# Optimization experiments

Measured on AMD Instinct MI355X. Metric: run time of the kernel, lower is better.

## Reference

```python
import jax, jax.numpy as jnp
import numpy as np
from jax import lax

D_MODEL = 1024
D_STATE = 16
D_CONV = 4
EXPAND = 2
D_INNER = EXPAND * D_MODEL          # 2048
DT_RANK = (D_MODEL + 15) // 16      # 64
FF_INNER = 4 * D_MODEL              # 4096
B, L = 2, 2048
EPS = 1e-5


def _layer_norm(x, g, b):
    mu = jnp.mean(x, axis=-1, keepdims=True)
    var = jnp.mean(jnp.square(x - mu), axis=-1, keepdims=True)
    return (x - mu) * lax.rsqrt(var + EPS) * g + b


def setup_inputs() -> dict:
    key = jax.random.key(0)
    ks = jax.random.split(key, 10)
    def n(k, shape, s=0.02):
        return jax.random.normal(k, shape, dtype=jnp.float32) * s
    x = jax.random.normal(ks[0], (B, L, D_MODEL), dtype=jnp.float32)
    return dict(
        x=x,
        ln1_g=jnp.ones((D_MODEL,), jnp.float32), ln1_b=jnp.zeros((D_MODEL,), jnp.float32),
        w_in=n(ks[1], (D_MODEL, 2 * D_INNER)),
        conv_w=n(ks[2], (D_INNER, D_CONV), 0.2), conv_b=jnp.zeros((D_INNER,), jnp.float32),
        w_x=n(ks[3], (D_INNER, DT_RANK + 2 * D_STATE)),
        w_dt=n(ks[4], (DT_RANK, D_INNER), 0.1),
        b_dt=jnp.full((D_INNER,), -4.6, jnp.float32),  # softplus(-4.6) ~= 0.01 dt init
        a_log=jnp.log(jnp.broadcast_to(jnp.arange(1, D_STATE + 1, dtype=jnp.float32), (D_INNER, D_STATE))),
        d_skip=jnp.ones((D_INNER,), jnp.float32),
        w_out=n(ks[5], (D_INNER, D_MODEL)),
        ln2_g=jnp.ones((D_MODEL,), jnp.float32), ln2_b=jnp.zeros((D_MODEL,), jnp.float32),
        w_ff1=n(ks[6], (D_MODEL, 2 * FF_INNER)), b_ff1=jnp.zeros((2 * FF_INNER,), jnp.float32),
        w_ff2=n(ks[7], (FF_INNER, D_MODEL)), b_ff2=jnp.zeros((D_MODEL,), jnp.float32),
    )


def _mamba(h, w_in, conv_w, conv_b, w_x, w_dt, b_dt, a_log, d_skip, w_out):
    # h: (B, L, D_MODEL)
    xz = h @ w_in                                   # (B, L, 2*D_INNER)
    xc, z = jnp.split(xz, 2, axis=-1)               # each (B, L, D_INNER)
    # depthwise causal conv1d along L
    xc_t = jnp.transpose(xc, (0, 2, 1))             # (B, D_INNER, L)
    xc_t = lax.conv_general_dilated(
        xc_t, conv_w[:, None, :], window_strides=(1,), padding=[(D_CONV - 1, 0)],
        feature_group_count=D_INNER, dimension_numbers=('NCH', 'OIH', 'NCH'))
    xc = jnp.transpose(xc_t, (0, 2, 1)) + conv_b
    xc = jax.nn.silu(xc)
    # input-dependent dt, B, C
    dbc = xc @ w_x                                  # (B, L, DT_RANK+2*D_STATE)
    dt_lo, Bm, Cm = jnp.split(dbc, [DT_RANK, DT_RANK + D_STATE], axis=-1)
    dt = jax.nn.softplus(dt_lo @ w_dt + b_dt)       # (B, L, D_INNER)
    A = -jnp.exp(a_log)                             # (D_INNER, D_STATE)

    def step(hst, inp):
        dt_t, B_t, C_t, x_t = inp                   # (B,di),(B,N),(B,N),(B,di)
        dA = jnp.exp(dt_t[..., None] * A)           # (B, D_INNER, D_STATE)
        hst = hst * dA + (dt_t * x_t)[..., None] * B_t[:, None, :]
        y = jnp.einsum('bdn,bn->bd', hst, C_t)
        return hst, y

    h0 = jnp.zeros((h.shape[0], D_INNER, D_STATE), dt.dtype)
    xs = (jnp.swapaxes(dt, 0, 1), jnp.swapaxes(Bm, 0, 1),
          jnp.swapaxes(Cm, 0, 1), jnp.swapaxes(xc, 0, 1))
    _, ys = lax.scan(step, h0, xs)                  # ys: (L, B, D_INNER)
    y = jnp.swapaxes(ys, 0, 1) + d_skip * xc
    y = y * jax.nn.silu(z)
    return y @ w_out                                # (B, L, D_MODEL)


def _geglu_ff(h, w1, b1, w2, b2):
    p = h @ w1 + b1
    a, g = jnp.split(p, 2, axis=-1)
    return (a * jax.nn.gelu(g)) @ w2 + b2


def reference(x, ln1_g, ln1_b, w_in, conv_w, conv_b, w_x, w_dt, b_dt, a_log,
              d_skip, w_out, ln2_g, ln2_b, w_ff1, b_ff1, w_ff2, b_ff2):
    h = _layer_norm(x, ln1_g, ln1_b)
    x = x + _mamba(h, w_in, conv_w, conv_b, w_x, w_dt, b_dt, a_log, d_skip, w_out)
    h2 = _layer_norm(x, ln2_g, ln2_b)
    x = x + _geglu_ff(h2, w_ff1, b_ff1, w_ff2, b_ff2)
    return x
```

## Files before the change

kernel.cpp:

```cpp
#include <hip/hip_runtime.h>
#include <hip/hip_bf16.h>
#include <stdint.h>
#include <stddef.h>


typedef __bf16 bf16;
typedef __bf16 bf16x8 __attribute__((ext_vector_type(8)));
typedef float  f32x4  __attribute__((ext_vector_type(4)));

static constexpr int kB  = 2;
static constexpr int kL  = 2048;
static constexpr int kDM = 1024;
static constexpr int kDI = 2048;
static constexpr int kM  = kB * kL;
static constexpr int kNC = 64;
static constexpr int kCH = kL / kNC;

__device__ __forceinline__ void gload16(const void* g, void* l) {
  __builtin_amdgcn_global_load_lds((__attribute__((address_space(1))) void*)g,
                                   (__attribute__((address_space(3))) void*)l,
                                   16, 0, 0);
}

__global__ __launch_bounds__(256) void transpose_to_bf16(
    const float* __restrict__ w, bf16* __restrict__ wt, int K, int N, int Npad) {
  __shared__ float t[32][33];
  const int k0 = blockIdx.x * 32, n0 = blockIdx.y * 32;
  const int tx = threadIdx.x & 31, ty = threadIdx.x >> 5;
#pragma unroll
  for (int i = ty; i < 32; i += 8) {
    float v = 0.f;
    if (k0 + i < K && n0 + tx < N) v = w[(size_t)(k0 + i) * N + n0 + tx];
    t[i][tx] = v;
  }
  __syncthreads();
#pragma unroll
  for (int i = ty; i < 32; i += 8) {
    const int n = n0 + i, k = k0 + tx;
    if (n < Npad && k < K) wt[(size_t)n * K + k] = (bf16)t[tx][i];
  }
}

__global__ __launch_bounds__(256) void layernorm_to_bf16(
    const float* __restrict__ x, const float* __restrict__ g,
    const float* __restrict__ b, bf16* __restrict__ out) {
  const int row = blockIdx.x;
  const float4 v = ((const float4*)(x + (size_t)row * kDM))[threadIdx.x];
  float s  = v.x + v.y + v.z + v.w;
  float s2 = v.x * v.x + v.y * v.y + v.z * v.z + v.w * v.w;
#pragma unroll
  for (int off = 1; off < 64; off <<= 1) {
    s  += __shfl_xor(s, off);
    s2 += __shfl_xor(s2, off);
  }
  __shared__ float ws[4], ws2[4];
  const int wave = threadIdx.x >> 6, lane = threadIdx.x & 63;
  if (lane == 0) { ws[wave] = s; ws2[wave] = s2; }
  __syncthreads();
  s  = ws[0] + ws[1] + ws[2] + ws[3];
  s2 = ws2[0] + ws2[1] + ws2[2] + ws2[3];
  const float mu  = s * (1.f / kDM);
  const float var = s2 * (1.f / kDM) - mu * mu;
  const float r   = rsqrtf(var + 1e-5f);
  const int c = threadIdx.x * 4;
  const float4 gg = ((const float4*)g)[threadIdx.x];
  const float4 bb = ((const float4*)b)[threadIdx.x];
  bf16* o = out + (size_t)row * kDM + c;
  o[0] = (bf16)((v.x - mu) * r * gg.x + bb.x);
  o[1] = (bf16)((v.y - mu) * r * gg.y + bb.y);
  o[2] = (bf16)((v.z - mu) * r * gg.z + bb.z);
  o[3] = (bf16)((v.w - mu) * r * gg.w + bb.w);
}

template <int MODE>
__global__ __launch_bounds__(256, 2) void gemm_bt(
    const bf16* __restrict__ A, int lda,
    const bf16* __restrict__ BT, int ldbt, int K,
    float* __restrict__ C0, bf16* __restrict__ C1,
    const float* __restrict__ bias, const float* __restrict__ res) {
  __shared__ __align__(16) bf16 As[128 * 32];
  __shared__ __align__(16) bf16 Bs[128 * 32];

  const int tid  = threadIdx.x;
  const int wave = tid >> 6;
  const int lane = tid & 63;
  const int m0 = blockIdx.y * 128;
  const int n0 = blockIdx.x * 128;
  const int wr = wave >> 1, wc = wave & 1;
  const int lr = lane & 15, kg = lane >> 4;

  const int srow = lane >> 2;
  const int scol = (lane & 3) * 8;

  const bf16* Ag0 = A  + (size_t)(m0 + wave * 32 + srow) * lda  + scol;
  const bf16* Ag1 = Ag0 + (size_t)16 * lda;
  const bf16* Bg0 = BT + (size_t)(n0 + wave * 32 + srow) * ldbt + scol;
  const bf16* Bg1 = Bg0 + (size_t)16 * ldbt;
  bf16* Al0 = As + wave * 1024;
  bf16* Al1 = Al0 + 512;
  bf16* Bl0 = Bs + wave * 1024;
  bf16* Bl1 = Bl0 + 512;

  f32x4 acc[4][4] = {};

  for (int kt = 0; kt < K; kt += 32) {
    __syncthreads();
    gload16(Ag0 + kt, Al0);
    gload16(Ag1 + kt, Al1);
    gload16(Bg0 + kt, Bl0);
    gload16(Bg1 + kt, Bl1);
    __syncthreads();

    bf16x8 af[4], bfr[4];
#pragma unroll
    for (int i = 0; i < 4; ++i) {
      af[i]  = *(const bf16x8*)(As + (wr * 64 + i * 16 + lr) * 32 + kg * 8);
      bfr[i] = *(const bf16x8*)(Bs + (wc * 64 + i * 16 + lr) * 32 + kg * 8);
    }
#pragma unroll
    for (int i = 0; i < 4; ++i)
#pragma unroll
      for (int j = 0; j < 4; ++j)
        acc[i][j] =
            __builtin_amdgcn_mfma_f32_16x16x32_bf16(af[i], bfr[j], acc[i][j], 0, 0, 0);
  }

#pragma unroll
  for (int i = 0; i < 4; ++i) {
    const int mbase = m0 + wr * 64 + i * 16 + kg * 4;
#pragma unroll
    for (int j = 0; j < 4; ++j) {
      const int n = n0 + wc * 64 + j * 16 + lr;
#pragma unroll
      for (int e = 0; e < 4; ++e) {
        const int m = mbase + e;
        const float v = acc[i][j][e];
        if constexpr (MODE == 0) {
          if (n < kDI) C0[(size_t)m * kDI + n] = v;
          else         C1[(size_t)m * kDI + (n - kDI)] = (bf16)(v / (1.f + expf(-v)));
        } else if constexpr (MODE == 1) {
          C0[(size_t)m * 128 + n] = v;
          if (n < 64) C1[(size_t)m * 64 + n] = (bf16)v;
        } else if constexpr (MODE == 2) {
          const float t = v + bias[n];
          const float sp = (t > 0.f) ? (t + log1pf(expf(-t))) : log1pf(expf(t));
          C0[(size_t)m * kDI + n] = sp;
        } else if constexpr (MODE == 3) {
          C0[(size_t)m * kDM + n] = v + res[(size_t)m * kDM + n];
        } else if constexpr (MODE == 4) {
          C1[(size_t)m * 8192 + n] = (bf16)(v + bias[n]);
        } else {
          C0[(size_t)m * kDM + n] = v + bias[n] + res[(size_t)m * kDM + n];
        }
      }
    }
  }
}

__global__ __launch_bounds__(256) void conv_silu(
    const float* __restrict__ xc_raw, const float* __restrict__ cw,
    const float* __restrict__ cb, float* __restrict__ xf, bf16* __restrict__ xb) {
  const int idx = blockIdx.x * 256 + threadIdx.x;
  const int d = idx & (kDI - 1);
  const int m = idx >> 11;
  const int l = m & (kL - 1);
  float acc = cb[d];
  const float w0 = cw[d * 4 + 0], w1 = cw[d * 4 + 1], w2 = cw[d * 4 + 2],
              w3 = cw[d * 4 + 3];
  if (l >= 3) acc += xc_raw[(size_t)(m - 3) * kDI + d] * w0;
  if (l >= 2) acc += xc_raw[(size_t)(m - 2) * kDI + d] * w1;
  if (l >= 1) acc += xc_raw[(size_t)(m - 1) * kDI + d] * w2;
  acc += xc_raw[(size_t)m * kDI + d] * w3;
  const float a = acc / (1.f + expf(-acc));
  xf[idx] = a;
  xb[idx] = (bf16)a;
}


__global__ __launch_bounds__(256) void scan_p1(
    const float* __restrict__ dt, const float* __restrict__ xc,
    const float* __restrict__ dbc, const float* __restrict__ a_log,
    float* __restrict__ P, float* __restrict__ Q) {
  const int dg = blockIdx.x & 7;
  const int c  = (blockIdx.x >> 3) & (kNC - 1);
  const int b  = blockIdx.x >> 9;
  const int d  = dg * 256 + threadIdx.x;
  __shared__ __align__(16) float BC[kCH][32];
  {
    const int l  = threadIdx.x >> 3;
    const int cg = (threadIdx.x & 7) * 4;
    *(float4*)&BC[l][cg] =
        *(const float4*)&dbc[(size_t)(b * kL + c * kCH + l) * 128 + 64 + cg];
  }
  __syncthreads();
  float A[16];
#pragma unroll
  for (int q = 0; q < 4; ++q) {
    const float4 al = *(const float4*)&a_log[d * 16 + q * 4];
    A[q * 4 + 0] = -__expf(al.x);
    A[q * 4 + 1] = -__expf(al.y);
    A[q * 4 + 2] = -__expf(al.z);
    A[q * 4 + 3] = -__expf(al.w);
  }
  float h[16] = {};
  float sdt = 0.f;
  const size_t rb = ((size_t)b * kL + c * kCH) * kDI + d;
#pragma unroll 2
  for (int l = 0; l < kCH; ++l) {
    const float dtv = dt[rb + (size_t)l * kDI];
    const float xv  = xc[rb + (size_t)l * kDI];
    const float u   = dtv * xv;
    sdt += dtv;
    float Bv[16];
    *(float4*)&Bv[0]  = *(const float4*)&BC[l][0];
    *(float4*)&Bv[4]  = *(const float4*)&BC[l][4];
    *(float4*)&Bv[8]  = *(const float4*)&BC[l][8];
    *(float4*)&Bv[12] = *(const float4*)&BC[l][12];
#pragma unroll
    for (int n = 0; n < 16; ++n) {
      const float dA = __expf(dtv * A[n]);
      h[n] = h[n] * dA + u * Bv[n];
    }
  }
  const size_t o = (((size_t)b * kNC + c) * kDI + d) * 16;
  float Pv[16];
#pragma unroll
  for (int n = 0; n < 16; ++n) Pv[n] = __expf(sdt * A[n]);
#pragma unroll
  for (int q = 0; q < 4; ++q) {
    *(float4*)&P[o + q * 4] = *(float4*)&Pv[q * 4];
    *(float4*)&Q[o + q * 4] = *(float4*)&h[q * 4];
  }
}

__global__ __launch_bounds__(256) void scan_p2(
    const float* __restrict__ P, const float* __restrict__ Q,
    float* __restrict__ H0) {
  const int i  = blockIdx.x * 256 + threadIdx.x;
  const int dn = i & (kDI * 16 - 1);
  const int b  = i >> 15;
  float h = 0.f;
#pragma unroll 8
  for (int c = 0; c < kNC; ++c) {
    const size_t idx = ((size_t)(b * kNC + c)) * (kDI * 16) + dn;
    H0[idx] = h;
    h = P[idx] * h + Q[idx];
  }
}

__global__ __launch_bounds__(256) void scan_p3(
    const float* __restrict__ dt, const float* __restrict__ xc,
    const float* __restrict__ dbc, const float* __restrict__ a_log,
    const float* __restrict__ d_skip, const bf16* __restrict__ zs,
    const float* __restrict__ H0, bf16* __restrict__ y) {
  const int dg = blockIdx.x & 7;
  const int c  = (blockIdx.x >> 3) & (kNC - 1);
  const int b  = blockIdx.x >> 9;
  const int d  = dg * 256 + threadIdx.x;
  __shared__ __align__(16) float BC[kCH][32];
  {
    const int l  = threadIdx.x >> 3;
    const int cg = (threadIdx.x & 7) * 4;
    *(float4*)&BC[l][cg] =
        *(const float4*)&dbc[(size_t)(b * kL + c * kCH + l) * 128 + 64 + cg];
  }
  __syncthreads();
  float A[16];
#pragma unroll
  for (int q = 0; q < 4; ++q) {
    const float4 al = *(const float4*)&a_log[d * 16 + q * 4];
    A[q * 4 + 0] = -__expf(al.x);
    A[q * 4 + 1] = -__expf(al.y);
    A[q * 4 + 2] = -__expf(al.z);
    A[q * 4 + 3] = -__expf(al.w);
  }
  const float dsk = d_skip[d];
  float h[16];
  const size_t o = (((size_t)b * kNC + c) * kDI + d) * 16;
#pragma unroll
  for (int q = 0; q < 4; ++q)
    *(float4*)&h[q * 4] = *(const float4*)&H0[o + q * 4];
  const size_t rb = ((size_t)b * kL + c * kCH) * kDI + d;
#pragma unroll 2
  for (int l = 0; l < kCH; ++l) {
    const size_t r  = rb + (size_t)l * kDI;
    const float dtv = dt[r];
    const float xv  = xc[r];
    const float zv  = (float)zs[r];
    const float u   = dtv * xv;
    float Bv[16], Cv[16];
    *(float4*)&Bv[0]  = *(const float4*)&BC[l][0];
    *(float4*)&Bv[4]  = *(const float4*)&BC[l][4];
    *(float4*)&Bv[8]  = *(const float4*)&BC[l][8];
    *(float4*)&Bv[12] = *(const float4*)&BC[l][12];
    *(float4*)&Cv[0]  = *(const float4*)&BC[l][16];
    *(float4*)&Cv[4]  = *(const float4*)&BC[l][20];
    *(float4*)&Cv[8]  = *(const float4*)&BC[l][24];
    *(float4*)&Cv[12] = *(const float4*)&BC[l][28];
    float pp[4] = {0.f, 0.f, 0.f, 0.f};
#pragma unroll
    for (int n = 0; n < 16; ++n) {
      const float dA = __expf(dtv * A[n]);
      h[n] = h[n] * dA + u * Bv[n];
      pp[n & 3] += h[n] * Cv[n];
    }
    const float part = (pp[0] + pp[1]) + (pp[2] + pp[3]);
    y[r] = (bf16)((part + dsk * xv) * zv);
  }
}

__global__ __launch_bounds__(256) void geglu(
    const bf16* __restrict__ p, bf16* __restrict__ v) {
  const int idx = blockIdx.x * 256 + threadIdx.x;
  const int m = idx >> 12, n = idx & 4095;
  const float a = (float)p[(size_t)m * 8192 + n];
  const float g = (float)p[(size_t)m * 8192 + 4096 + n];
  const float g3 = g * g * g;
  const float t  = tanhf(0.7978845608028654f * (g + 0.044715f * g3));
  v[idx] = (bf16)(a * (0.5f * g * (1.f + t)));
}

extern "C" void kernel_launch(void* const* d_in, const int* in_sizes, int n_in,
                              void* d_out, int out_size, void* d_ws, size_t ws_size,
                              hipStream_t stream) {
  const float* x      = (const float*)d_in[0];
  const float* ln1_g  = (const float*)d_in[1];
  const float* ln1_b  = (const float*)d_in[2];
  const float* w_in   = (const float*)d_in[3];
  const float* conv_w = (const float*)d_in[4];
  const float* conv_b = (const float*)d_in[5];
  const float* w_x    = (const float*)d_in[6];
  const float* w_dt   = (const float*)d_in[7];
  const float* b_dt   = (const float*)d_in[8];
  const float* a_log  = (const float*)d_in[9];
  const float* d_skip = (const float*)d_in[10];
  const float* w_out  = (const float*)d_in[11];
  const float* ln2_g  = (const float*)d_in[12];
  const float* ln2_b  = (const float*)d_in[13];
  const float* w_ff1  = (const float*)d_in[14];
  const float* b_ff1  = (const float*)d_in[15];
  const float* w_ff2  = (const float*)d_in[16];
  const float* b_ff2  = (const float*)d_in[17];
  float* out = (float*)d_out;
  char* ws = (char*)d_ws;

  bf16* wT_in  = (bf16*)(ws + 0);
  bf16* wT_x   = (bf16*)(ws + 8388608);
  bf16* wT_dt  = (bf16*)(ws + 8912896);
  bf16* wT_out = (bf16*)(ws + 9175040);
  bf16* wT_ff1 = (bf16*)(ws + 13369344);
  bf16* wT_ff2 = (bf16*)(ws + 30146560);
  bf16* h_bf   = (bf16*)(ws + 38535168);
  float* xcraw = (float*)(ws + 46923776);
  bf16* zs     = (bf16*)(ws + 80478208);
  float* xcf   = (float*)(ws + 97255424);
  bf16* xcb    = (bf16*)(ws + 130809856);
  float* dbc   = (float*)(ws + 147587072);
  bf16* dtlo   = (bf16*)(ws + 149684224);
  bf16* pbuf   = (bf16*)(ws + 150208512);
  float* dtbuf = xcraw;
  bf16*  vbuf  = (bf16*)xcraw;
  float* out1  = (float*)zs;
  bf16*  ybuf  = xcb;
  bf16*  h2    = h_bf;
  float* Pbuf  = (float*)pbuf;
  float* Qbuf  = (float*)((char*)pbuf + (16 << 20));
  float* H0buf = (float*)((char*)pbuf + (32 << 20));

  const dim3 tb(256);
  transpose_to_bf16<<<dim3(32, 128), tb, 0, stream>>>(w_in, wT_in, 1024, 4096, 4096);
  transpose_to_bf16<<<dim3(64, 4), tb, 0, stream>>>(w_x, wT_x, 2048, 96, 128);
  transpose_to_bf16<<<dim3(2, 64), tb, 0, stream>>>(w_dt, wT_dt, 64, 2048, 2048);
  transpose_to_bf16<<<dim3(64, 32), tb, 0, stream>>>(w_out, wT_out, 2048, 1024, 1024);
  transpose_to_bf16<<<dim3(32, 256), tb, 0, stream>>>(w_ff1, wT_ff1, 1024, 8192, 8192);
  transpose_to_bf16<<<dim3(128, 32), tb, 0, stream>>>(w_ff2, wT_ff2, 4096, 1024, 1024);

  layernorm_to_bf16<<<kM, tb, 0, stream>>>(x, ln1_g, ln1_b, h_bf);

  gemm_bt<0><<<dim3(32, 32), tb, 0, stream>>>(h_bf, 1024, wT_in, 1024, 1024,
                                              xcraw, zs, nullptr, nullptr);
  conv_silu<<<(kM * kDI) / 256, tb, 0, stream>>>(xcraw, conv_w, conv_b, xcf, xcb);

  gemm_bt<1><<<dim3(1, 32), tb, 0, stream>>>(xcb, 2048, wT_x, 2048, 2048,
                                             dbc, dtlo, nullptr, nullptr);
  gemm_bt<2><<<dim3(16, 32), tb, 0, stream>>>(dtlo, 64, wT_dt, 64, 64,
                                              dtbuf, nullptr, b_dt, nullptr);

  scan_p1<<<kB * kNC * (kDI / 256), tb, 0, stream>>>(dtbuf, xcf, dbc, a_log,
                                                     Pbuf, Qbuf);
  scan_p2<<<(kB * kDI * 16) / 256, tb, 0, stream>>>(Pbuf, Qbuf, H0buf);
  scan_p3<<<kB * kNC * (kDI / 256), tb, 0, stream>>>(dtbuf, xcf, dbc, a_log,
                                                     d_skip, zs, H0buf, ybuf);

  gemm_bt<3><<<dim3(8, 32), tb, 0, stream>>>(ybuf, 2048, wT_out, 2048, 2048,
                                             out1, nullptr, nullptr, x);
  layernorm_to_bf16<<<kM, tb, 0, stream>>>(out1, ln2_g, ln2_b, h2);

  gemm_bt<4><<<dim3(64, 32), tb, 0, stream>>>(h2, 1024, wT_ff1, 1024, 1024,
                                              nullptr, pbuf, b_ff1, nullptr);
  geglu<<<(kM * 4096) / 256, tb, 0, stream>>>(pbuf, vbuf);

  gemm_bt<5><<<dim3(8, 32), tb, 0, stream>>>(vbuf, 4096, wT_ff2, 4096, 4096,
                                             out, nullptr, b_ff2, out1);
  (void)in_sizes; (void)n_in; (void)out_size; (void)ws_size;
}
```

Before: 687.9 us.

## Apply split-K to low-occupancy GEMMs with separate reduction kernels

The x-projection, output-projection and FF2 GEMMs launched few blocks (32 or 256) relative to the GPU's compute units. They now split K across blockIdx.z (8, 2 and 4 ways) and write fp32 partials into a scratch buffer. New reduction kernels sum the partials and apply the residual and bias epilogues. This raises parallelism at the cost of extra partial-sum memory traffic and additional kernel launches.

```diff
diff --git a/kernel.cpp b/kernel.cpp
--- a/kernel.cpp
+++ b/kernel.cpp
@@ -86,15 +86,16 @@
   const int lane = tid & 63;
   const int m0 = blockIdx.y * 128;
   const int n0 = blockIdx.x * 128;
+  const int kz = blockIdx.z * K;
   const int wr = wave >> 1, wc = wave & 1;
   const int lr = lane & 15, kg = lane >> 4;
 
   const int srow = lane >> 2;
   const int scol = (lane & 3) * 8;
 
-  const bf16* Ag0 = A  + (size_t)(m0 + wave * 32 + srow) * lda  + scol;
+  const bf16* Ag0 = A  + (size_t)(m0 + wave * 32 + srow) * lda  + scol + kz;
   const bf16* Ag1 = Ag0 + (size_t)16 * lda;
-  const bf16* Bg0 = BT + (size_t)(n0 + wave * 32 + srow) * ldbt + scol;
+  const bf16* Bg0 = BT + (size_t)(n0 + wave * 32 + srow) * ldbt + scol + kz;
   const bf16* Bg1 = Bg0 + (size_t)16 * ldbt;
   bf16* Al0 = As + wave * 1024;
   bf16* Al1 = Al0 + 512;
@@ -138,23 +139,61 @@
         if constexpr (MODE == 0) {
           if (n < kDI) C0[(size_t)m * kDI + n] = v;
           else         C1[(size_t)m * kDI + (n - kDI)] = (bf16)(v / (1.f + expf(-v)));
-        } else if constexpr (MODE == 1) {
-          C0[(size_t)m * 128 + n] = v;
-          if (n < 64) C1[(size_t)m * 64 + n] = (bf16)v;
         } else if constexpr (MODE == 2) {
           const float t = v + bias[n];
           const float sp = (t > 0.f) ? (t + log1pf(expf(-t))) : log1pf(expf(t));
           C0[(size_t)m * kDI + n] = sp;
-        } else if constexpr (MODE == 3) {
-          C0[(size_t)m * kDM + n] = v + res[(size_t)m * kDM + n];
         } else if constexpr (MODE == 4) {
           C1[(size_t)m * 8192 + n] = (bf16)(v + bias[n]);
+        } else if constexpr (MODE == 6) {
+          C0[((size_t)blockIdx.z * kM + m) * 1024 + n] = v;
         } else {
-          C0[(size_t)m * kDM + n] = v + bias[n] + res[(size_t)m * kDM + n];
+          C0[((size_t)blockIdx.z * kM + m) * 128 + n] = v;
         }
       }
     }
   }
+}
+
+__global__ __launch_bounds__(256) void reduce_dbc(
+    const float* __restrict__ P, float* __restrict__ dbc, bf16* __restrict__ dtlo) {
+  const int i = blockIdx.x * 256 + threadIdx.x;
+  float s = 0.f;
+#pragma unroll
+  for (int z = 0; z < 8; ++z) s += P[(size_t)z * (kM * 128) + i];
+  dbc[i] = s;
+  const int n = i & 127;
+  if (n < 64) dtlo[(size_t)(i >> 7) * 64 + n] = (bf16)s;
+}
+
+__global__ __launch_bounds__(256) void reduce_wout(
+    const float* __restrict__ P, const float* __restrict__ x,
+    float* __restrict__ o) {
+  const size_t i = ((size_t)blockIdx.x * 256 + threadIdx.x) * 4;
+  const float4 a  = *(const float4*)&x[i];
+  const float4 p0 = *(const float4*)&P[i];
+  const float4 p1 = *(const float4*)&P[(size_t)kM * 1024 + i];
+  float4 r;
+  r.x = a.x + p0.x + p1.x;  r.y = a.y + p0.y + p1.y;
+  r.z = a.z + p0.z + p1.z;  r.w = a.w + p0.w + p1.w;
+  *(float4*)&o[i] = r;
+}
+
+__global__ __launch_bounds__(256) void reduce_ff2(
+    const float* __restrict__ P, const float* __restrict__ o1,
+    const float* __restrict__ bias, float* __restrict__ o) {
+  const size_t i = ((size_t)blockIdx.x * 256 + threadIdx.x) * 4;
+  const int n = (int)(i & 1023);
+  const float4 a  = *(const float4*)&o1[i];
+  const float4 bb = *(const float4*)&bias[n];
+  float4 s;
+  s.x = a.x + bb.x;  s.y = a.y + bb.y;  s.z = a.z + bb.z;  s.w = a.w + bb.w;
+#pragma unroll
+  for (int z = 0; z < 4; ++z) {
+    const float4 p = *(const float4*)&P[(size_t)z * (kM * 1024) + i];
+    s.x += p.x;  s.y += p.y;  s.z += p.z;  s.w += p.w;
+  }
+  *(float4*)&o[i] = s;
 }
 
 __global__ __launch_bounds__(256) void conv_silu(
@@ -175,7 +214,6 @@
   xf[idx] = a;
   xb[idx] = (bf16)a;
 }
-
 
 __global__ __launch_bounds__(256) void scan_p1(
     const float* __restrict__ dt, const float* __restrict__ xc,
@@ -363,6 +401,7 @@
   float* out1  = (float*)zs;
   bf16*  ybuf  = xcb;
   bf16*  h2    = h_bf;
+  float* Part  = (float*)pbuf;
   float* Pbuf  = (float*)pbuf;
   float* Qbuf  = (float*)((char*)pbuf + (16 << 20));
   float* H0buf = (float*)((char*)pbuf + (32 << 20));
@@ -381,8 +420,10 @@
                                               xcraw, zs, nullptr, nullptr);
   conv_silu<<<(kM * kDI) / 256, tb, 0, stream>>>(xcraw, conv_w, conv_b, xcf, xcb);
 
-  gemm_bt<1><<<dim3(1, 32), tb, 0, stream>>>(xcb, 2048, wT_x, 2048, 2048,
-                                             dbc, dtlo, nullptr, nullptr);
+  gemm_bt<7><<<dim3(1, 32, 8), tb, 0, stream>>>(xcb, 2048, wT_x, 2048, 256,
+                                                Part, nullptr, nullptr, nullptr);
+  reduce_dbc<<<(kM * 128) / 256, tb, 0, stream>>>(Part, dbc, dtlo);
+
   gemm_bt<2><<<dim3(16, 32), tb, 0, stream>>>(dtlo, 64, wT_dt, 64, 64,
                                               dtbuf, nullptr, b_dt, nullptr);
 
@@ -392,15 +433,18 @@
   scan_p3<<<kB * kNC * (kDI / 256), tb, 0, stream>>>(dtbuf, xcf, dbc, a_log,
                                                      d_skip, zs, H0buf, ybuf);
 
-  gemm_bt<3><<<dim3(8, 32), tb, 0, stream>>>(ybuf, 2048, wT_out, 2048, 2048,
-                                             out1, nullptr, nullptr, x);
+  gemm_bt<6><<<dim3(8, 32, 2), tb, 0, stream>>>(ybuf, 2048, wT_out, 2048, 1024,
+                                                Part, nullptr, nullptr, nullptr);
+  reduce_wout<<<(kM * 1024) / 1024, tb, 0, stream>>>(Part, x, out1);
+
   layernorm_to_bf16<<<kM, tb, 0, stream>>>(out1, ln2_g, ln2_b, h2);
 
   gemm_bt<4><<<dim3(64, 32), tb, 0, stream>>>(h2, 1024, wT_ff1, 1024, 1024,
                                               nullptr, pbuf, b_ff1, nullptr);
   geglu<<<(kM * 4096) / 256, tb, 0, stream>>>(pbuf, vbuf);
 
-  gemm_bt<5><<<dim3(8, 32), tb, 0, stream>>>(vbuf, 4096, wT_ff2, 4096, 4096,
-                                             out, nullptr, b_ff2, out1);
+  gemm_bt<6><<<dim3(8, 32, 4), tb, 0, stream>>>(vbuf, 4096, wT_ff2, 4096, 1024,
+                                                Part, nullptr, nullptr, nullptr);
+  reduce_ff2<<<(kM * 1024) / 1024, tb, 0, stream>>>(Part, out1, b_ff2, out);
   (void)in_sizes; (void)n_in; (void)out_size; (void)ws_size;
 }
```

Result: slower. 749.6 us (+9.0%).
